# Kernel optimization log

Hardware: AMD Instinct MI355X
Metric: run time of the kernel (lower is better)

The kernel has to match this reference:

```python
import jax, jax.numpy as jnp
import numpy as np

HIDDEN = 1024
HEADS = 16
HEAD_DIM = HIDDEN // HEADS


def setup_inputs() -> dict:
    key = jax.random.key(0)
    ks = jax.random.split(key, 9)
    s = 1.0 / np.sqrt(HIDDEN)
    return {
        "x": jax.random.normal(ks[0], (2, 2048, HIDDEN), dtype=jnp.float32),
        "Wq": jax.random.uniform(ks[1], (HIDDEN, HIDDEN), jnp.float32, -s, s),
        "bq": jax.random.uniform(ks[2], (HIDDEN,), jnp.float32, -s, s),
        "Wk": jax.random.uniform(ks[3], (HIDDEN, HIDDEN), jnp.float32, -s, s),
        "bk": jax.random.uniform(ks[4], (HIDDEN,), jnp.float32, -s, s),
        "Wv": jax.random.uniform(ks[5], (HIDDEN, HIDDEN), jnp.float32, -s, s),
        "bv": jax.random.uniform(ks[6], (HIDDEN,), jnp.float32, -s, s),
        "Wo": jax.random.uniform(ks[7], (HIDDEN, HIDDEN), jnp.float32, -s, s),
        "bo": jax.random.uniform(ks[8], (HIDDEN,), jnp.float32, -s, s),
    }


def reference(x, Wq, bq, Wk, bk, Wv, bv, Wo, bo):
    B, N, C = x.shape
    H, D = HEADS, HEAD_DIM
    # torch Linear: y = x @ W.T + b; weights here stored as (out, in)
    q = (x @ Wq.T + bq).reshape(B, N, H, D).transpose(0, 2, 1, 3)  # bhnd
    k = (x @ Wk.T + bk).reshape(B, N, H, D).transpose(0, 2, 1, 3)
    v = (x @ Wv.T + bv).reshape(B, N, H, D).transpose(0, 2, 1, 3)
    scale = D ** -0.5
    attn = jnp.einsum("bhnd,bhmd->bhnm", q, k) * scale
    attn = jax.nn.softmax(attn, axis=-1)
    out = jnp.einsum("bhnm,bhmd->bhnd", attn, v)
    out = out.transpose(0, 2, 1, 3).reshape(B, N, C)
    return out @ Wo.T + bo
```

## Files before the change

kernel.cpp:

```cpp
#include <hip/hip_runtime.h>
#include <stdint.h>

#define HIDDEN 1024
#define HEADS 16
#define HEAD_DIM 64
#define NBATCH 2
#define SEQ 2048

typedef short bh8 __attribute__((ext_vector_type(8)));
typedef _Float16 hf4 __attribute__((ext_vector_type(4)));
typedef _Float16 hf8 __attribute__((ext_vector_type(8)));
typedef float fx4 __attribute__((ext_vector_type(4)));

#define MFMA_BF16(a, b, c) __builtin_amdgcn_mfma_f32_16x16x32_bf16((a), (b), (c), 0, 0, 0)
#define MFMA_F16_16(a, b, c) __builtin_amdgcn_mfma_f32_16x16x16f16((a), (b), (c), 0, 0, 0)

__device__ __forceinline__ short f2bf(float f) {
  union { float f; uint32_t u; } v; v.f = f;
  uint32_t r = v.u + 0x7fffu + ((v.u >> 16) & 1u);
  return (short)(r >> 16);
}
__device__ __forceinline__ short f2h(float f) {
  union { _Float16 h; short s; } v; v.h = (_Float16)f;
  return v.s;
}

typedef __attribute__((address_space(1))) void GV;
typedef __attribute__((address_space(3))) void LV;
__device__ __forceinline__ void gl_lds16(const void* g, void* l) {
  __builtin_amdgcn_global_load_lds((GV*)g, (LV*)l, 16, 0, 0);
}

__device__ __forceinline__ size_t img_off(int row, int k) {
  int rt = row >> 7, kt = k >> 6;
  int g = (((row & 127) >> 4) << 1) + ((k & 63) >> 5);
  int l = (((k & 31) >> 3) << 4) + (row & 15);
  return ((size_t)((rt * 16 + kt) * 16 + g) << 9) + (l << 3) + (k & 7);
}

__global__ void cvt_kernel(const float* __restrict__ x,
                           const float* __restrict__ wq, const float* __restrict__ wk,
                           const float* __restrict__ wv, const float* __restrict__ wo,
                           short* __restrict__ xb, short* __restrict__ wqb,
                           short* __restrict__ wkb, short* __restrict__ wvb,
                           short* __restrict__ wob) {
  long t = (long)blockIdx.x * blockDim.x + threadIdx.x;
  long i = t * 4;
  const float* s; short* d; long off;
  if (i < 4194304L) { s = x; d = xb; off = i; }
  else {
    long j = i - 4194304L;
    int w = (int)(j >> 20);
    off = j & 1048575L;
    s = (w == 0) ? wq : (w == 1) ? wk : (w == 2) ? wv : wo;
    d = (w == 0) ? wqb : (w == 1) ? wkb : (w == 2) ? wvb : wob;
  }
  float4 v = *(const float4*)(s + off);
  short4 o;
  o.x = f2bf(v.x); o.y = f2bf(v.y); o.z = f2bf(v.z); o.w = f2bf(v.w);
  int row = (int)(off >> 10), k = (int)(off & 1023);
  *(short4*)(d + img_off(row, k)) = o;
}

__global__ __launch_bounds__(256)
void qkv_kernel(const short* __restrict__ xb,
                const short* __restrict__ wqb, const short* __restrict__ wkb,
                const short* __restrict__ wvb,
                const float* __restrict__ bq, const float* __restrict__ bk,
                const float* __restrict__ bv,
                short* __restrict__ Q, short* __restrict__ K, short* __restrict__ Vt) {
  __shared__ __align__(16) short Alds[8192];
  __shared__ __align__(16) short Blds[8192];

  const int lin = blockIdx.x;
  const int xcd = lin & 7, idx = lin >> 3;
  const int mt = (xcd >> 1) * 8 + (idx & 7);
  const int zo = (xcd & 1) * 12 + (idx >> 3);
  const int z = zo >> 3, ot = zo & 7;

  const short* W = (z == 0) ? wqb : (z == 1) ? wkb : wvb;
  const float* bias = (z == 0) ? bq : (z == 1) ? bk : bv;
  const int tid = threadIdx.x;
  const int lane = tid & 63, w = tid >> 6;
  const int r = lane & 15, q = lane >> 4;
  const int wr = w >> 1, wc = w & 1;

  fx4 acc[4][4] = {};

  for (int kt = 0; kt < 16; ++kt) {
#pragma unroll
    for (int i = 0; i < 4; ++i) {
      int c = w * 4 + i;
      gl_lds16(xb + (((size_t)(mt * 16 + kt) * 16 + c) << 9) + lane * 8,
               (char*)Alds + c * 1024);
      gl_lds16(W + (((size_t)(ot * 16 + kt) * 16 + c) << 9) + lane * 8,
               (char*)Blds + c * 1024);
    }
    __syncthreads();
#pragma unroll
    for (int ks = 0; ks < 2; ++ks) {
      bh8 af[4], bf_[4];
#pragma unroll
      for (int ti = 0; ti < 4; ++ti)
        af[ti] = *(const bh8*)&Alds[(((wr * 4 + ti) * 2 + ks) << 9) + lane * 8];
#pragma unroll
      for (int tj = 0; tj < 4; ++tj)
        bf_[tj] = *(const bh8*)&Blds[(((wc * 4 + tj) * 2 + ks) << 9) + lane * 8];
#pragma unroll
      for (int ti = 0; ti < 4; ++ti)
#pragma unroll
        for (int tj = 0; tj < 4; ++tj)
          acc[ti][tj] = MFMA_BF16(af[ti], bf_[tj], acc[ti][tj]);
    }
    __syncthreads();
  }

  const float QS = 0.18033688011112042f;
#pragma unroll
  for (int ti = 0; ti < 4; ++ti)
#pragma unroll
    for (int tj = 0; tj < 4; ++tj)
#pragma unroll
      for (int i = 0; i < 4; ++i) {
        int row = mt * 128 + wr * 64 + ti * 16 + q * 4 + i;
        int col = ot * 128 + wc * 64 + tj * 16 + r;
        float v = acc[ti][tj][i] + bias[col];
        int b = row >> 11, n = row & 2047;
        int h = col >> 6, d = col & 63;
        int bh = b * 16 + h;
        size_t base = (size_t)bh * 131072;
        if (z == 0) {
          Q[base + (size_t)n * 64 + d] = f2bf(v * QS);
        } else if (z == 1) {
          int jj = n >> 7, rin = n & 127;
          int g = ((rin >> 4) * 2) + (d >> 5);
          int lp = (((d & 31) >> 3) * 16) + (rin & 15);
          K[base + jj * 8192 + g * 512 + lp * 8 + (d & 7)] = f2bf(v);
        } else {
          int jj = n >> 7, keyin = n & 127;
          int dt = d >> 4, rp = d & 15;
          int ks2 = keyin >> 4, pi = ks2 >> 1, hh = ks2 & 1;
          int qp = (keyin & 15) >> 2, ii = keyin & 3;
          Vt[base + jj * 8192 + (dt * 4 + pi) * 512 + (qp * 16 + rp) * 8 + hh * 4 + ii] = f2h(v);
        }
      }
}

__global__ __launch_bounds__(512, 4)
void attn_kernel(const short* __restrict__ Q, const short* __restrict__ Kf,
                 const short* __restrict__ Vf, short* __restrict__ A) {
  __shared__ __align__(16) short Klds[2][8192];
  __shared__ __align__(16) short Vlds[2][8192];

  const int lin = blockIdx.x;
  const int xcd = lin & 7, idx = lin >> 3;
  const int bh = xcd + 8 * (idx & 3);
  const int n0 = (idx >> 2) * 128;

  const int tid = threadIdx.x;
  const int lane = tid & 63, w = tid >> 6;
  const int r = lane & 15, q = lane >> 4;

  const short* Qg = Q + (size_t)bh * 131072;
  const short* Kg = Kf + (size_t)bh * 131072;
  const short* Vg = Vf + (size_t)bh * 131072;

  bh8 qf[2];
#pragma unroll
  for (int ks = 0; ks < 2; ++ks)
    qf[ks] = *(const bh8*)(Qg + (size_t)(n0 + w * 16 + r) * 64 + ks * 32 + q * 8);

  fx4 o[4] = {};
  float l_run = 0.f;

#define ATTN_STAGE(j, b)                                                        \
  {                                                                             \
    const short* ktp = Kg + (j) * 8192;                                         \
    const short* vtp = Vg + (j) * 8192;                                         \
    _Pragma("unroll") for (int i = 0; i < 4; ++i) {                             \
      if (w < 4) {                                                              \
        int c = w * 4 + i;                                                      \
        gl_lds16(ktp + c * 512 + lane * 8, (char*)&Klds[b][0] + c * 1024);      \
      } else {                                                                  \
        int c = (w - 4) * 4 + i;                                                \
        gl_lds16(vtp + c * 512 + lane * 8, (char*)&Vlds[b][0] + c * 1024);      \
      }                                                                         \
    }                                                                           \
  }

  ATTN_STAGE(0, 0);
  __syncthreads();

  for (int j = 0; j < 16; ++j) {
    int cur = j & 1;
    if (j < 15) ATTN_STAGE(j + 1, cur ^ 1);

    fx4 s[8] = {};
#pragma unroll
    for (int ks = 0; ks < 2; ++ks)
#pragma unroll
      for (int tj = 0; tj < 8; ++tj) {
        bh8 kf = *(const bh8*)&Klds[cur][(tj * 2 + ks) * 512 + lane * 8];
        s[tj] = MFMA_BF16(kf, qf[ks], s[tj]);
      }

    hf4 p[8];
#pragma unroll
    for (int tj = 0; tj < 8; ++tj)
#pragma unroll
      for (int i = 0; i < 4; ++i) {
        float e = __builtin_amdgcn_exp2f(s[tj][i]);
        l_run += e;
        p[tj][i] = (_Float16)e;
      }

#pragma unroll
    for (int pi = 0; pi < 4; ++pi)
#pragma unroll
      for (int dt = 0; dt < 4; ++dt) {
        hf8 vv = *(const hf8*)&Vlds[cur][(dt * 4 + pi) * 512 + lane * 8];
        hf4 vlo = __builtin_shufflevector(vv, vv, 0, 1, 2, 3);
        hf4 vhi = __builtin_shufflevector(vv, vv, 4, 5, 6, 7);
        o[dt] = MFMA_F16_16(vlo, p[2 * pi], o[dt]);
        o[dt] = MFMA_F16_16(vhi, p[2 * pi + 1], o[dt]);
      }
    __syncthreads();
  }
#undef ATTN_STAGE

  float l = l_run;
  l += __shfl_xor(l, 16);
  l += __shfl_xor(l, 32);
  const float inv = 1.0f / l;

  const int h = bh & 15;
  const int mt = (bh >> 4) * 16 + (n0 >> 7);
#pragma unroll
  for (int dt = 0; dt < 4; ++dt) {
    short4 ov;
    ov.x = f2bf(o[dt][0] * inv);
    ov.y = f2bf(o[dt][1] * inv);
    ov.z = f2bf(o[dt][2] * inv);
    ov.w = f2bf(o[dt][3] * inv);
    int g = w * 2 + (dt >> 1);
    int lp = ((dt & 1) * 2 + (q >> 1)) * 16 + r;
    *(short4*)(A + (((size_t)(mt * 16 + h) * 16 + g) << 9) + lp * 8 + (q & 1) * 4) = ov;
  }
}

__global__ __launch_bounds__(256)
void proj_kernel(const short* __restrict__ ab, const short* __restrict__ wob,
                 const float* __restrict__ bo, float* __restrict__ out) {
  __shared__ __align__(16) short Alds[8192];
  __shared__ __align__(16) short Blds[8192];

  const int lin = blockIdx.x;
  const int xcd = lin & 7, idx = lin >> 3;
  const int mt = (xcd >> 1) * 8 + (idx & 7);
  const int ot = (xcd & 1) * 4 + (idx >> 3);

  const int tid = threadIdx.x;
  const int lane = tid & 63, w = tid >> 6;
  const int r = lane & 15, q = lane >> 4;
  const int wr = w >> 1, wc = w & 1;

  fx4 acc[4][4] = {};

  for (int kt = 0; kt < 16; ++kt) {
#pragma unroll
    for (int i = 0; i < 4; ++i) {
      int c = w * 4 + i;
      gl_lds16(ab + (((size_t)(mt * 16 + kt) * 16 + c) << 9) + lane * 8,
               (char*)Alds + c * 1024);
      gl_lds16(wob + (((size_t)(ot * 16 + kt) * 16 + c) << 9) + lane * 8,
               (char*)Blds + c * 1024);
    }
    __syncthreads();
#pragma unroll
    for (int ks = 0; ks < 2; ++ks) {
      bh8 af[4], bf_[4];
#pragma unroll
      for (int ti = 0; ti < 4; ++ti)
        af[ti] = *(const bh8*)&Alds[(((wr * 4 + ti) * 2 + ks) << 9) + lane * 8];
#pragma unroll
      for (int tj = 0; tj < 4; ++tj)
        bf_[tj] = *(const bh8*)&Blds[(((wc * 4 + tj) * 2 + ks) << 9) + lane * 8];
#pragma unroll
      for (int ti = 0; ti < 4; ++ti)
#pragma unroll
        for (int tj = 0; tj < 4; ++tj)
          acc[ti][tj] = MFMA_BF16(af[ti], bf_[tj], acc[ti][tj]);
    }
    __syncthreads();
  }

#pragma unroll
  for (int ti = 0; ti < 4; ++ti)
#pragma unroll
    for (int tj = 0; tj < 4; ++tj)
#pragma unroll
      for (int i = 0; i < 4; ++i) {
        int row = mt * 128 + wr * 64 + ti * 16 + q * 4 + i;
        int col = ot * 128 + wc * 64 + tj * 16 + r;
        out[(size_t)row * 1024 + col] = acc[ti][tj][i] + bo[col];
      }
}

extern "C" void kernel_launch(void* const* d_in, const int* in_sizes, int n_in,
                              void* d_out, int out_size, void* d_ws, size_t ws_size,
                              hipStream_t stream) {
  const float* x  = (const float*)d_in[0];
  const float* Wq = (const float*)d_in[1];
  const float* bq = (const float*)d_in[2];
  const float* Wk = (const float*)d_in[3];
  const float* bk = (const float*)d_in[4];
  const float* Wv = (const float*)d_in[5];
  const float* bv = (const float*)d_in[6];
  const float* Wo = (const float*)d_in[7];
  const float* bo = (const float*)d_in[8];
  float* out = (float*)d_out;
  char* ws = (char*)d_ws;

  short* xb  = (short*)(ws);
  short* wqb = (short*)(ws + 8388608);
  short* wkb = (short*)(ws + 8388608 + 2097152);
  short* wvb = (short*)(ws + 8388608 + 2 * 2097152);
  short* wob = (short*)(ws + 8388608 + 3 * 2097152);
  short* Qb  = (short*)(ws + 16777216);
  short* Kb  = (short*)(ws + 16777216 + 8388608);
  short* Vtb = (short*)(ws + 16777216 + 2 * 8388608);
  short* Ab  = (short*)(ws);

  cvt_kernel<<<8192, 256, 0, stream>>>(x, Wq, Wk, Wv, Wo, xb, wqb, wkb, wvb, wob);
  qkv_kernel<<<768, 256, 0, stream>>>(xb, wqb, wkb, wvb, bq, bk, bv, Qb, Kb, Vtb);
  attn_kernel<<<512, 512, 0, stream>>>(Qb, Kb, Vtb, Ab);
  proj_kernel<<<256, 256, 0, stream>>>(Ab, wob, bo, out);
}
```

Before: 195.7 us.

## Widen conversion stores, stage QKV epilogue through LDS, shrink projection tiles

The conversion kernel now handles 8 elements per thread and writes 16-byte vectors, which halves the thread count and widens the stores. The QKV epilogue first writes its scattered 2-byte results into shared memory in the final swizzled layout, then copies each tile to global memory with coalesced 16-byte stores. The output projection moves from 128x128 to 64x64 tiles, which quadruples the grid so the GPU's compute units are better filled, at the cost of more redundant operand loads. Together these aim to cut uncoalesced write traffic and raise occupancy in the smaller GEMM.

```diff
diff --git a/kernel.cpp b/kernel.cpp
--- a/kernel.cpp
+++ b/kernel.cpp
@@ -45,7 +45,7 @@
                            short* __restrict__ wkb, short* __restrict__ wvb,
                            short* __restrict__ wob) {
   long t = (long)blockIdx.x * blockDim.x + threadIdx.x;
-  long i = t * 4;
+  long i = t * 8;
   const float* s; short* d; long off;
   if (i < 4194304L) { s = x; d = xb; off = i; }
   else {
@@ -55,11 +55,13 @@
     s = (w == 0) ? wq : (w == 1) ? wk : (w == 2) ? wv : wo;
     d = (w == 0) ? wqb : (w == 1) ? wkb : (w == 2) ? wvb : wob;
   }
-  float4 v = *(const float4*)(s + off);
-  short4 o;
-  o.x = f2bf(v.x); o.y = f2bf(v.y); o.z = f2bf(v.z); o.w = f2bf(v.w);
+  float4 v0 = *(const float4*)(s + off);
+  float4 v1 = *(const float4*)(s + off + 4);
+  bh8 o;
+  o[0] = f2bf(v0.x); o[1] = f2bf(v0.y); o[2] = f2bf(v0.z); o[3] = f2bf(v0.w);
+  o[4] = f2bf(v1.x); o[5] = f2bf(v1.y); o[6] = f2bf(v1.z); o[7] = f2bf(v1.w);
   int row = (int)(off >> 10), k = (int)(off & 1023);
-  *(short4*)(d + img_off(row, k)) = o;
+  *(bh8*)(d + img_off(row, k)) = o;
 }
 
 __global__ __launch_bounds__(256)
@@ -69,8 +71,9 @@
                 const float* __restrict__ bq, const float* __restrict__ bk,
                 const float* __restrict__ bv,
                 short* __restrict__ Q, short* __restrict__ K, short* __restrict__ Vt) {
-  __shared__ __align__(16) short Alds[8192];
-  __shared__ __align__(16) short Blds[8192];
+  __shared__ __align__(16) short smem[16384];
+  short* Alds = smem;
+  short* Blds = smem + 8192;
 
   const int lin = blockIdx.x;
   const int xcd = lin & 7, idx = lin >> 3;
@@ -122,28 +125,44 @@
     for (int tj = 0; tj < 4; ++tj)
 #pragma unroll
       for (int i = 0; i < 4; ++i) {
-        int row = mt * 128 + wr * 64 + ti * 16 + q * 4 + i;
-        int col = ot * 128 + wc * 64 + tj * 16 + r;
-        float v = acc[ti][tj][i] + bias[col];
-        int b = row >> 11, n = row & 2047;
-        int h = col >> 6, d = col & 63;
-        int bh = b * 16 + h;
-        size_t base = (size_t)bh * 131072;
+        int nl = wr * 64 + ti * 16 + q * 4 + i;
+        int cl = wc * 64 + tj * 16 + r;
+        int hl = cl >> 6, d = cl & 63;
+        float v = acc[ti][tj][i] + bias[ot * 128 + cl];
+        short sv; int lo;
         if (z == 0) {
-          Q[base + (size_t)n * 64 + d] = f2bf(v * QS);
+          sv = f2bf(v * QS);
+          lo = hl * 8192 + nl * 64 + d;
         } else if (z == 1) {
-          int jj = n >> 7, rin = n & 127;
-          int g = ((rin >> 4) * 2) + (d >> 5);
-          int lp = (((d & 31) >> 3) * 16) + (rin & 15);
-          K[base + jj * 8192 + g * 512 + lp * 8 + (d & 7)] = f2bf(v);
+          sv = f2bf(v);
+          int g = ((nl >> 4) << 1) + (d >> 5);
+          int lp = (((d & 31) >> 3) << 4) + (nl & 15);
+          lo = hl * 8192 + g * 512 + lp * 8 + (d & 7);
         } else {
-          int jj = n >> 7, keyin = n & 127;
+          sv = f2h(v);
           int dt = d >> 4, rp = d & 15;
-          int ks2 = keyin >> 4, pi = ks2 >> 1, hh = ks2 & 1;
-          int qp = (keyin & 15) >> 2, ii = keyin & 3;
-          Vt[base + jj * 8192 + (dt * 4 + pi) * 512 + (qp * 16 + rp) * 8 + hh * 4 + ii] = f2h(v);
+          int ks2 = nl >> 4, pi = ks2 >> 1, hh = ks2 & 1;
+          int qp = (nl & 15) >> 2, ii = nl & 3;
+          lo = hl * 8192 + (dt * 4 + pi) * 512 + (qp * 16 + rp) * 8 + hh * 4 + ii;
         }
-      }
+        smem[lo] = sv;
+      }
+  __syncthreads();
+  {
+    int b = mt >> 4;
+    int n0 = (mt & 15) * 128;
+    int jj = mt & 15;
+    short* dst = (z == 0) ? Q : (z == 1) ? K : Vt;
+#pragma unroll
+    for (int kk = 0; kk < 8; ++kk) {
+      int s = kk * 256 + tid;
+      int hl = s >> 10, inner = s & 1023;
+      int bh = b * 16 + ot * 2 + hl;
+      size_t go = (size_t)bh * 131072 +
+                  (z == 0 ? (size_t)n0 * 64 : (size_t)jj * 8192) + (size_t)inner * 8;
+      *(int4*)(dst + go) = *(const int4*)(smem + (size_t)s * 8);
+    }
+  }
 }
 
 __global__ __launch_bounds__(512, 4)
@@ -251,58 +270,60 @@
 __global__ __launch_bounds__(256)
 void proj_kernel(const short* __restrict__ ab, const short* __restrict__ wob,
                  const float* __restrict__ bo, float* __restrict__ out) {
-  __shared__ __align__(16) short Alds[8192];
-  __shared__ __align__(16) short Blds[8192];
+  __shared__ __align__(16) short Alds[4096];
+  __shared__ __align__(16) short Blds[4096];
 
   const int lin = blockIdx.x;
   const int xcd = lin & 7, idx = lin >> 3;
-  const int mt = (xcd >> 1) * 8 + (idx & 7);
-  const int ot = (xcd & 1) * 4 + (idx >> 3);
+  const int mt = xcd * 8 + (idx & 7);
+  const int ot = idx >> 3;
 
   const int tid = threadIdx.x;
   const int lane = tid & 63, w = tid >> 6;
   const int r = lane & 15, q = lane >> 4;
-  const int wr = w >> 1, wc = w & 1;
-
-  fx4 acc[4][4] = {};
+  const int wm = w & 1, wn = w >> 1;
+  const int rt = mt >> 1, rh = mt & 1;
+  const int st = ot >> 1, sh = ot & 1;
+
+  fx4 acc[2][2] = {};
 
   for (int kt = 0; kt < 16; ++kt) {
 #pragma unroll
-    for (int i = 0; i < 4; ++i) {
-      int c = w * 4 + i;
-      gl_lds16(ab + (((size_t)(mt * 16 + kt) * 16 + c) << 9) + lane * 8,
+    for (int i = 0; i < 2; ++i) {
+      int c = w * 2 + i;
+      gl_lds16(ab + (((size_t)(rt * 16 + kt) * 16 + rh * 8 + c) << 9) + lane * 8,
                (char*)Alds + c * 1024);
-      gl_lds16(wob + (((size_t)(ot * 16 + kt) * 16 + c) << 9) + lane * 8,
+      gl_lds16(wob + (((size_t)(st * 16 + kt) * 16 + sh * 8 + c) << 9) + lane * 8,
                (char*)Blds + c * 1024);
     }
     __syncthreads();
 #pragma unroll
     for (int ks = 0; ks < 2; ++ks) {
-      bh8 af[4], bf_[4];
-#pragma unroll
-      for (int ti = 0; ti < 4; ++ti)
-        af[ti] = *(const bh8*)&Alds[(((wr * 4 + ti) * 2 + ks) << 9) + lane * 8];
-#pragma unroll
-      for (int tj = 0; tj < 4; ++tj)
-        bf_[tj] = *(const bh8*)&Blds[(((wc * 4 + tj) * 2 + ks) << 9) + lane * 8];
-#pragma unroll
-      for (int ti = 0; ti < 4; ++ti)
-#pragma unroll
-        for (int tj = 0; tj < 4; ++tj)
-          acc[ti][tj] = MFMA_BF16(af[ti], bf_[tj], acc[ti][tj]);
-    }
-    __syncthreads();
-  }
-
-#pragma unroll
-  for (int ti = 0; ti < 4; ++ti)
-#pragma unroll
-    for (int tj = 0; tj < 4; ++tj)
+      bh8 af[2], bf_[2];
+#pragma unroll
+      for (int tm = 0; tm < 2; ++tm)
+        af[tm] = *(const bh8*)&Alds[(((wm * 2 + tm) * 2 + ks) << 9) + lane * 8];
+#pragma unroll
+      for (int tn = 0; tn < 2; ++tn)
+        bf_[tn] = *(const bh8*)&Blds[(((wn * 2 + tn) * 2 + ks) << 9) + lane * 8];
+#pragma unroll
+      for (int tm = 0; tm < 2; ++tm)
+#pragma unroll
+        for (int tn = 0; tn < 2; ++tn)
+          acc[tm][tn] = MFMA_BF16(af[tm], bf_[tn], acc[tm][tn]);
+    }
+    __syncthreads();
+  }
+
+#pragma unroll
+  for (int tm = 0; tm < 2; ++tm)
+#pragma unroll
+    for (int tn = 0; tn < 2; ++tn)
 #pragma unroll
       for (int i = 0; i < 4; ++i) {
-        int row = mt * 128 + wr * 64 + ti * 16 + q * 4 + i;
-        int col = ot * 128 + wc * 64 + tj * 16 + r;
-        out[(size_t)row * 1024 + col] = acc[ti][tj][i] + bo[col];
+        int row = mt * 64 + wm * 32 + tm * 16 + q * 4 + i;
+        int col = ot * 64 + wn * 32 + tn * 16 + r;
+        out[(size_t)row * 1024 + col] = acc[tm][tn][i] + bo[col];
       }
 }
 
@@ -331,8 +352,8 @@
   short* Vtb = (short*)(ws + 16777216 + 2 * 8388608);
   short* Ab  = (short*)(ws);
 
-  cvt_kernel<<<8192, 256, 0, stream>>>(x, Wq, Wk, Wv, Wo, xb, wqb, wkb, wvb, wob);
+  cvt_kernel<<<4096, 256, 0, stream>>>(x, Wq, Wk, Wv, Wo, xb, wqb, wkb, wvb, wob);
   qkv_kernel<<<768, 256, 0, stream>>>(xb, wqb, wkb, wvb, bq, bk, bv, Qb, Kb, Vtb);
   attn_kernel<<<512, 512, 0, stream>>>(Qb, Kb, Vtb, Ab);
-  proj_kernel<<<256, 256, 0, stream>>>(Ab, wob, bo, out);
-}
+  proj_kernel<<<1024, 256, 0, stream>>>(Ab, wob, bo, out);
+}
```

New measurement: 198.4 us. About the same (+1.4%).
